# Performance work log

Hardware: AMD Instinct MI355X
Metric: run time of the kernel (lower is better)

## Reference

```python
import jax, jax.numpy as jnp
import numpy as np
import math

N, E, C, NB, NEL, NG = 8192, 131072, 64, 8, 4, 16
R_MAX, AVG_NEI, P_CUT, NL, SH = 5.0, 16.0, 6, 2, 16


def _sph(u):
    # real spherical harmonics l=0..3, component normalization (sum_m Y_lm^2 = 2l+1 on unit sphere)
    x, y, z = u[:, 0], u[:, 1], u[:, 2]
    s3, s15, s5 = math.sqrt(3.0), math.sqrt(15.0), math.sqrt(5.0)
    s105, s7 = math.sqrt(105.0), math.sqrt(7.0)
    c35, c21 = math.sqrt(35.0 / 8.0), math.sqrt(21.0 / 8.0)
    Y = [jnp.ones_like(x),
         s3 * x, s3 * y, s3 * z,
         s15 * x * y, s15 * y * z, 0.5 * s5 * (3 * z * z - 1), s15 * x * z, 0.5 * s15 * (x * x - y * y),
         c35 * y * (3 * x * x - y * y), s105 * x * y * z, c21 * y * (5 * z * z - 1),
         0.5 * s7 * (5 * z ** 3 - 3 * z), c21 * x * (5 * z * z - 1),
         0.5 * s105 * z * (x * x - y * y), c35 * x * (x * x - 3 * y * y)]
    return jnp.stack(Y, axis=-1)  # [E,16]


def _bessel(r):
    k = jnp.arange(1, NB + 1, dtype=r.dtype)
    return math.sqrt(2.0 / R_MAX) * jnp.sin(k * jnp.pi * r[:, None] / R_MAX) / r[:, None]


def _poly_cutoff(r):
    p = float(P_CUT)
    x = r / R_MAX
    f = (1.0 - 0.5 * (p + 1) * (p + 2) * x ** p + p * (p + 2) * x ** (p + 1)
         - 0.5 * p * (p + 1) * x ** (p + 2))
    return f * (x < 1.0)


def setup_inputs() -> dict:
    key = jax.random.key(0)
    ks = jax.random.split(key, 16)
    sc = lambda fan: 1.0 / math.sqrt(fan)
    return {
        "pos": 2.0 * jax.random.normal(ks[0], (N, 3), jnp.float32),
        "atom_types": jax.random.randint(ks[1], (N,), 0, NEL),
        "edge_index": jax.random.randint(ks[2], (2, E), 0, N),
        "batch": jnp.sort(jax.random.randint(ks[3], (N,), 0, NG)),
        "W_embed": jax.random.normal(ks[4], (NEL, C), jnp.float32),
        "W_r1": sc(NB) * jax.random.normal(ks[5], (NL, NB, 64), jnp.float32),
        "W_r2": sc(64) * jax.random.normal(ks[6], (NL, 64, 64), jnp.float32),
        "W_r3": sc(64) * jax.random.normal(ks[7], (NL, 64, C), jnp.float32),
        "W_sc": sc(C) * jax.random.normal(ks[8], (NL, NEL, C, C), jnp.float32),
        "w_prod": 0.5 * jax.random.normal(ks[9], (NL, NEL, 4), jnp.float32),
        "w_ro0": sc(C) * jax.random.normal(ks[10], (C,), jnp.float32),
        "W_ro1a": sc(C) * jax.random.normal(ks[11], (C, 16), jnp.float32),
        "w_ro1b": sc(16) * jax.random.normal(ks[12], (16,), jnp.float32),
    }


def reference(pos, atom_types, edge_index, batch, W_embed, W_r1, W_r2, W_r3,
              W_sc, w_prod, w_ro0, W_ro1a, w_ro1b):
    src, dst = edge_index[0], edge_index[1]
    vec = pos[dst] - pos[src]                      # [E,3]
    r = jnp.sqrt(jnp.sum(vec * vec, -1) + 1e-12)   # [E]
    Y = _sph(vec / r[:, None])                     # [E,SH]
    edge_feats = _bessel(r) * _poly_cutoff(r)[:, None]  # [E,NB]
    h = W_embed[atom_types]                        # one-hot @ W == lookup, [N,C]
    energies = [jnp.zeros((NG,), pos.dtype)]       # pair_repulsion disabled
    for i in range(NL):
        Rw = jax.nn.silu(edge_feats @ W_r1[i])
        Rw = jax.nn.silu(Rw @ W_r2[i])
        Rw = Rw @ W_r3[i]                          # radial MLP weights [E,C]
        # gather-TP-scatter: message [E,C,SH] -> node A [N,C,SH]
        m = (Rw * h[src])[:, :, None] * Y[:, None, :]
        A = jax.ops.segment_sum(m.reshape(E, C * SH), dst,
                                num_segments=N).reshape(N, C, SH) / AVG_NEI
        sc_feat = jnp.einsum('nc,ncd->nd', h, W_sc[i][atom_types])  # element-dep skip
        inv = jnp.stack([A[:, :, 0],
                         jnp.sum(A[:, :, 1:4] ** 2, -1),
                         jnp.sum(A[:, :, 4:9] ** 2, -1),
                         jnp.sum(A[:, :, 9:16] ** 2, -1)], axis=-1)  # [N,C,4]
        h = jnp.einsum('ncj,nj->nc', inv, w_prod[i][atom_types]) + sc_feat
        if i < NL - 1:
            e_node = h @ w_ro0                     # linear readout
        else:
            e_node = jax.nn.silu(h @ W_ro1a) @ w_ro1b  # gated MLP readout
        energies.append(jax.ops.segment_sum(e_node, batch, num_segments=NG))
    contributions = jnp.stack(energies, -1)        # [NG, NL+1]
    return jnp.sum(contributions, -1)              # total energy per graph
```

## Files before the change

kernel.cpp:

```cpp
#include <hip/hip_runtime.h>
#include <hip/hip_bf16.h>
#include <math.h>

#define N_NODES 8192
#define N_EDGES 131072
#define NGRP 16
#define NLAY 2
#define NELM 4
constexpr float INV_AVG = 1.0f / 16.0f;
constexpr float PI_F = 3.14159265358979323846f;

#define CV_POS   0
#define CV_EMB   24576
#define CV_SC    42240
#define CV_PROD  75008
#define CV_RO0   75040
#define CV_RO1A  75104
#define CV_RO1B  76128
#define CVT_N    76144

#define SWZ_PER_L 10240
#define SWZ_N     20480

#define B_CVT  230
#define B_SWZ  80
#define B_HIST 512
#define CVT_WORK 58736

typedef __hip_bfloat16 bf16;
typedef __attribute__((ext_vector_type(8))) short bf16x8;
typedef __attribute__((ext_vector_type(4))) float f32x4;

__device__ __forceinline__ float silu_f(float x){ return x / (1.0f + __expf(-x)); }
__device__ __forceinline__ float bfbits2f(unsigned short u){
  return __uint_as_float(((unsigned)u) << 16);
}
__device__ __forceinline__ void unpack2(unsigned u, float& lo, float& hi){
  lo = __uint_as_float(u << 16);
  hi = __uint_as_float(u & 0xffff0000u);
}
__device__ __forceinline__ short f2bs(float v){
  union { bf16 b; short s; } u; u.b = __float2bfloat16(v); return u.s;
}
__device__ __forceinline__ float ldf(const void* p, int i, int flag){
  if (flag) return bfbits2f(((const unsigned short*)p)[i]);
  return ((const float*)p)[i];
}
__device__ __forceinline__ int detect_fl(const void* pos){
  int lane = threadIdx.x & 63;
  const unsigned short* u = (const unsigned short*)pos;
  float va = bfbits2f(u[2*lane]), vb = bfbits2f(u[2*lane+1]);
  bool bad = !(fabsf(va) <= 1000.0f) || !(fabsf(vb) <= 1000.0f);
  return (__ballot(bad) == 0ull) ? 1 : 0;
}
__device__ __forceinline__ void WSYNC(){ __builtin_amdgcn_wave_barrier(); }

__device__ __forceinline__ void gl_lds4(const void* g, void* l){
  __builtin_amdgcn_global_load_lds(
      (const __attribute__((address_space(1))) unsigned*)g,
      (__attribute__((address_space(3))) unsigned*)l, 4, 0, 0);
}
__device__ __forceinline__ void gl_lds16(const void* g, void* l){
  __builtin_amdgcn_global_load_lds(
      (const __attribute__((address_space(1))) unsigned*)g,
      (__attribute__((address_space(3))) unsigned*)l, 16, 0, 0);
}

__global__ void k_setup1(const void* __restrict__ pos, const void* __restrict__ Wemb,
                         const void* __restrict__ Wsc, const void* __restrict__ wprod,
                         const void* __restrict__ wro0, const void* __restrict__ Wro1a,
                         const void* __restrict__ wro1b, const void* __restrict__ Wr1,
                         const void* __restrict__ Wr2, const void* __restrict__ Wr3,
                         const int* __restrict__ dstp, float* __restrict__ cv,
                         short* __restrict__ swz, int* __restrict__ deg){
  int b = blockIdx.x, tix = threadIdx.x;
  if (b >= B_CVT + B_SWZ){
    int e = (b - B_CVT - B_SWZ)*256 + tix;
    atomicAdd(&deg[dstp[e]], 1);
    return;
  }
  int fl = detect_fl(pos);
  if (b < B_CVT){
    int i = b*256 + tix;
    if (i < 24576){ cv[CV_POS + i] = ldf(pos, i, fl); return; }
    if (i < 24832){ int j=i-24576; cv[CV_EMB + j] = ldf(Wemb, j, fl); return; }
    if (i < 57600){ int j=i-24832; cv[CV_SC  + j] = ldf(Wsc,  j, fl); return; }
    if (i < 57632){ int j=i-57600; cv[CV_PROD+ j] = ldf(wprod,j, fl); return; }
    if (i < 57696){ int j=i-57632; cv[CV_RO0 + j] = ldf(wro0, j, fl); return; }
    if (i < 58720){ int j=i-57696; cv[CV_RO1A+ j] = ldf(Wro1a,j, fl); return; }
    if (i < CVT_WORK){ int j=i-58720; cv[CV_RO1B+ j] = ldf(wro1b,j, fl); return; }
    return;
  }
  int i = (b - B_CVT)*256 + tix;
  int l = i / SWZ_PER_L, w = i % SWZ_PER_L;
  float v;
  if (w < 2048){
    int t = w >> 9, q = (w >> 7) & 3, n = (w >> 3) & 15, j = w & 7;
    int k = q*8 + j;
    v = (k < 8) ? ldf(Wr1, l*512 + k*64 + t*16 + n, fl) : 0.0f;
  } else if (w < 6144){
    int w2 = w - 2048;
    int nt = w2 >> 10, kt = (w2 >> 9) & 1, q = (w2 >> 7) & 3, n = (w2 >> 3) & 15, j = w2 & 7;
    int k = kt*32 + q*8 + j;
    v = ldf(Wr2, l*4096 + k*64 + nt*16 + n, fl);
  } else {
    int w3 = w - 6144;
    int nt = w3 >> 10, kt = (w3 >> 9) & 1, q = (w3 >> 7) & 3, n = (w3 >> 3) & 15, j = w3 & 7;
    int k = kt*32 + q*8 + j;
    v = ldf(Wr3, l*4096 + k*64 + nt*16 + n, fl);
  }
  swz[i] = f2bs(v);
}

__global__ void k_setup2(const int* __restrict__ deg, int* __restrict__ row_start,
                         int* __restrict__ cursor, const int* __restrict__ types,
                         const float* __restrict__ cvemb, float* __restrict__ h,
                         float* __restrict__ ene){
  if (blockIdx.x == 0){
    __shared__ int lds[1024];
    int t = threadIdx.x;
    if (t < NGRP) ene[t] = 0.0f;
    int v[8]; int tot = 0;
#pragma unroll
    for (int k = 0; k < 8; k++){ v[k] = deg[t*8+k]; tot += v[k]; }
    lds[t] = tot; __syncthreads();
    for (int off = 1; off < 1024; off <<= 1){
      int x = (t >= off) ? lds[t-off] : 0;
      __syncthreads();
      lds[t] += x;
      __syncthreads();
    }
    int base = lds[t] - tot;
#pragma unroll
    for (int k = 0; k < 8; k++){ row_start[t*8+k] = base; cursor[t*8+k] = base; base += v[k]; }
    if (t == 1023) row_start[N_NODES] = base;
  } else {
    int i = (blockIdx.x - 1)*1024 + threadIdx.x;
    int n = i >> 6, c = i & 63;
    h[i] = cvemb[types[n]*64 + c];
  }
}

__global__ void k_fillgeom(const int* __restrict__ ei, int* __restrict__ cursor,
                           const float* __restrict__ posf, int* __restrict__ sslot,
                           unsigned short* __restrict__ Yb, float* __restrict__ rbuf){
  int e = blockIdx.x*256 + threadIdx.x;
  int s = ei[e], d = ei[N_EDGES + e];
  int slot = atomicAdd(&cursor[d], 1);
  sslot[slot] = s;
  float vx = posf[d*3+0] - posf[s*3+0];
  float vy = posf[d*3+1] - posf[s*3+1];
  float vz = posf[d*3+2] - posf[s*3+2];
  float r = sqrtf(vx*vx + vy*vy + vz*vz + 1e-12f);
  float ir = 1.0f / r;
  float x = vx*ir, y = vy*ir, z = vz*ir;
  const float s3 = 1.7320508075688772f, s15 = 3.872983346207417f, s5 = 2.23606797749979f;
  const float s105 = 10.246950765959598f, s7 = 2.6457513110645907f;
  const float c35 = 2.091650066335189f, c21 = 1.6201851746019651f;
  float x2 = x*x, y2 = y*y, z2 = z*z;
  float ys[16] = {
    1.0f, s3*x, s3*y, s3*z,
    s15*x*y, s15*y*z, 0.5f*s5*(3.0f*z2-1.0f), s15*x*z,
    0.5f*s15*(x2-y2), c35*y*(3.0f*x2-y2), s105*x*y*z, c21*y*(5.0f*z2-1.0f),
    0.5f*s7*(5.0f*z2*z-3.0f*z), c21*x*(5.0f*z2-1.0f), 0.5f*s105*z*(x2-y2),
    c35*x*(x2-3.0f*y2) };
  union { bf16 b[16]; uint4 u[2]; } pk;
#pragma unroll
  for (int k = 0; k < 16; k++) pk.b[k] = __float2bfloat16(ys[k]);
  uint4* yp = (uint4*)(Yb + (size_t)slot*16);
  yp[0] = pk.u[0];
  yp[1] = pk.u[1];
  rbuf[slot] = r;
}

#define ROWS 72
__global__ void __launch_bounds__(256) k_mlp2(const float* __restrict__ rbuf,
        const short* __restrict__ sw, bf16* __restrict__ Rwb){
  __shared__ short lds[4][16*ROWS];
  int tix = threadIdx.x;
  int wv = tix >> 6, lane = tix & 63;
  int q = lane >> 4, nn = lane & 15;
  int ebase = blockIdx.x*64 + wv*16;

  float r = rbuf[ebase + nn];
  float xc = r * 0.2f;
  float f = 0.0f;
  if (xc < 1.0f){
    float x3 = xc*xc*xc, x6 = x3*x3, x7 = x6*xc, x8 = x7*xc;
    f = 1.0f - 28.0f*x6 + 48.0f*x7 - 21.0f*x8;
  }
  float bs = 0.6324555320336759f * f / r;
  float t0 = PI_F * r * 0.2f;
  float ef[8];
#pragma unroll
  for (int k = 0; k < 8; k++) ef[k] = bs * __sinf((float)(k+1) * t0);

  bf16x8 af1 = {0,0,0,0,0,0,0,0};
  if (q == 0){
#pragma unroll
    for (int j = 0; j < 8; j++) af1[j] = f2bs(ef[j]);
  }
  short* A = lds[wv];
  int row = lane >> 2, c4 = lane & 3;

  for (int l = 0; l < NLAY; l++){
    const bf16x8* S1 = (const bf16x8*)(sw + l*SWZ_PER_L);
    const bf16x8* S2 = (const bf16x8*)(sw + l*SWZ_PER_L + 2048);
    const bf16x8* S3 = (const bf16x8*)(sw + l*SWZ_PER_L + 6144);
    f32x4 acc[4];
#pragma unroll
    for (int t = 0; t < 4; t++){
      bf16x8 b = S1[t*64 + q*16 + nn];
      f32x4 z = {0.f,0.f,0.f,0.f};
      acc[t] = __builtin_amdgcn_mfma_f32_16x16x32_bf16(af1, b, z, 0, 0, 0);
    }
#pragma unroll
    for (int t = 0; t < 4; t++)
#pragma unroll
      for (int rg = 0; rg < 4; rg++)
        A[(q*4+rg)*ROWS + t*16 + nn] = f2bs(silu_f(acc[t][rg]));
    WSYNC();

    bf16x8 a0 = *(const bf16x8*)&A[nn*ROWS + 0*32 + q*8];
    bf16x8 a1 = *(const bf16x8*)&A[nn*ROWS + 1*32 + q*8];
    WSYNC();
#pragma unroll
    for (int t = 0; t < 4; t++){
      f32x4 z = {0.f,0.f,0.f,0.f};
      bf16x8 b0 = S2[t*128 + 0*64 + q*16 + nn];
      bf16x8 b1 = S2[t*128 + 1*64 + q*16 + nn];
      z = __builtin_amdgcn_mfma_f32_16x16x32_bf16(a0, b0, z, 0, 0, 0);
      z = __builtin_amdgcn_mfma_f32_16x16x32_bf16(a1, b1, z, 0, 0, 0);
      acc[t] = z;
    }
#pragma unroll
    for (int t = 0; t < 4; t++)
#pragma unroll
      for (int rg = 0; rg < 4; rg++)
        A[(q*4+rg)*ROWS + t*16 + nn] = f2bs(silu_f(acc[t][rg]));
    WSYNC();

    a0 = *(const bf16x8*)&A[nn*ROWS + 0*32 + q*8];
    a1 = *(const bf16x8*)&A[nn*ROWS + 1*32 + q*8];
    WSYNC();
#pragma unroll
    for (int t = 0; t < 4; t++){
      f32x4 z = {0.f,0.f,0.f,0.f};
      bf16x8 b0 = S3[t*128 + 0*64 + q*16 + nn];
      bf16x8 b1 = S3[t*128 + 1*64 + q*16 + nn];
      z = __builtin_amdgcn_mfma_f32_16x16x32_bf16(a0, b0, z, 0, 0, 0);
      z = __builtin_amdgcn_mfma_f32_16x16x32_bf16(a1, b1, z, 0, 0, 0);
      acc[t] = z;
    }
#pragma unroll
    for (int t = 0; t < 4; t++)
#pragma unroll
      for (int rg = 0; rg < 4; rg++)
        A[(q*4+rg)*ROWS + t*16 + nn] = f2bs(acc[t][rg]);
    WSYNC();

    uint4 u0 = *(const uint4*)&A[row*ROWS + c4*16];
    uint4 u1 = *(const uint4*)&A[row*ROWS + c4*16 + 8];
    uint4* gp = (uint4*)((unsigned short*)Rwb + (size_t)l*N_EDGES*64
                         + ((size_t)(ebase + row))*64 + c4*16);
    gp[0] = u0;
    gp[1] = u1;
    WSYNC();
  }
}

template<int LAYER_KIND>
__global__ void __launch_bounds__(256) k_gu(const bf16* __restrict__ Rwb,
        const float* __restrict__ h_old, float* __restrict__ h_new,
        const unsigned short* __restrict__ Yb, const int* __restrict__ row_start,
        const int* __restrict__ sslot,
        const int* __restrict__ types, const float* __restrict__ Wsc,
        const float* __restrict__ wprod, const float* __restrict__ wro0,
        const float* __restrict__ Wro1a, const float* __restrict__ wro1b,
        const int* __restrict__ batch, float* __restrict__ ene){
  __shared__ __align__(16) float          hS[4][16][64];
  __shared__ __align__(16) unsigned short rwS[4][16][64];
  __shared__ __align__(16) unsigned short yS[4][16][16];
  __shared__ float ebins[NGRP];
  __shared__ float hn_l[4][64];
  int tix = threadIdx.x;
  if (tix < NGRP) ebins[tix] = 0.0f;
  __syncthreads();
  int wv = tix >> 6, lane = tix & 63;
  int n = blockIdx.x * 4 + wv;
  int beg = row_start[n], end = row_start[n + 1];
  const unsigned short* RW = (const unsigned short*)Rwb;

  float acc[16];
#pragma unroll
  for (int s = 0; s < 16; s++) acc[s] = 0.0f;

  for (int cb = beg; cb < end; cb += 16){
    int cnt = min(16, end - cb);
    WSYNC();
    int sv = sslot[min(cb + (lane & 15), N_EDGES - 1)];
    const char* rwsrc = (const char*)RW + (size_t)cb*128 + lane*16;
    gl_lds16(rwsrc,        &rwS[wv][0][0]);
    gl_lds16(rwsrc + 1024, &rwS[wv][8][0]);
    const char* ysrc = (const char*)Yb + (size_t)cb*32 + lane*4;
    gl_lds4(ysrc,       &yS[wv][0][0]);
    gl_lds4(ysrc + 256, &yS[wv][8][0]);
    for (int i = 0; i < cnt; i++){
      int src = __builtin_amdgcn_readlane(sv, i);
      gl_lds4(h_old + (size_t)src*64 + lane, &hS[wv][i][0]);
    }
    asm volatile("s_waitcnt vmcnt(0)" ::: "memory");
    __builtin_amdgcn_sched_barrier(0);
    for (int i = 0; i < cnt; i++){
      float g = hS[wv][i][lane] * bfbits2f(rwS[wv][i][lane]);
      const uint4* yq = (const uint4*)&yS[wv][i][0];
      uint4 ya = yq[0], yb = yq[1];
      float lo, hi;
      unpack2(ya.x, lo, hi); acc[0]  += g*lo; acc[1]  += g*hi;
      unpack2(ya.y, lo, hi); acc[2]  += g*lo; acc[3]  += g*hi;
      unpack2(ya.z, lo, hi); acc[4]  += g*lo; acc[5]  += g*hi;
      unpack2(ya.w, lo, hi); acc[6]  += g*lo; acc[7]  += g*hi;
      unpack2(yb.x, lo, hi); acc[8]  += g*lo; acc[9]  += g*hi;
      unpack2(yb.y, lo, hi); acc[10] += g*lo; acc[11] += g*hi;
      unpack2(yb.z, lo, hi); acc[12] += g*lo; acc[13] += g*hi;
      unpack2(yb.w, lo, hi); acc[14] += g*lo; acc[15] += g*hi;
    }
  }
#pragma unroll
  for (int s = 0; s < 16; s++) acc[s] *= INV_AVG;

  int ty = __builtin_amdgcn_readfirstlane(types[n]);
  const float* Ws = Wsc + (size_t)ty*4096;
  float sc0 = 0.f, sc1 = 0.f, sc2 = 0.f, sc3 = 0.f;
#pragma unroll
  for (int c = 0; c < 64; c += 4){
    sc0 += h_old[(size_t)n*64 + c+0] * Ws[(c+0)*64 + lane];
    sc1 += h_old[(size_t)n*64 + c+1] * Ws[(c+1)*64 + lane];
    sc2 += h_old[(size_t)n*64 + c+2] * Ws[(c+2)*64 + lane];
    sc3 += h_old[(size_t)n*64 + c+3] * Ws[(c+3)*64 + lane];
  }
  float sc = (sc0 + sc1) + (sc2 + sc3);

  float inv0 = acc[0];
  float inv1 = acc[1]*acc[1] + acc[2]*acc[2] + acc[3]*acc[3];
  float inv2 = acc[4]*acc[4] + acc[5]*acc[5] + acc[6]*acc[6] + acc[7]*acc[7]
             + acc[8]*acc[8];
  float inv3 = acc[9]*acc[9] + acc[10]*acc[10] + acc[11]*acc[11] + acc[12]*acc[12]
             + acc[13]*acc[13] + acc[14]*acc[14] + acc[15]*acc[15];
  const float* wp = wprod + ty*4;
  float hn = inv0*wp[0] + inv1*wp[1] + inv2*wp[2] + inv3*wp[3] + sc;
  h_new[(size_t)n*64 + lane] = hn;

  float ev;
  if (LAYER_KIND == 0){
    float p = hn * wro0[lane];
#pragma unroll
    for (int off = 32; off >= 1; off >>= 1) p += __shfl_xor(p, off, 64);
    ev = p;
  } else {
    hn_l[wv][lane] = hn;
    int j = lane & 15;
    float pj = 0.0f;
#pragma unroll
    for (int c = 0; c < 64; c++)
      pj += hn_l[wv][c] * Wro1a[c*16 + j];
    float evj = silu_f(pj) * wro1b[j];
    evj += __shfl_xor(evj, 8, 64);
    evj += __shfl_xor(evj, 4, 64);
    evj += __shfl_xor(evj, 2, 64);
    evj += __shfl_xor(evj, 1, 64);
    ev = evj;
  }
  if (lane == 0) atomicAdd(&ebins[batch[n]], ev);
  __syncthreads();
  if (tix < NGRP){
    float v = ebins[tix];
    if (v != 0.0f) atomicAdd(&ene[tix], v);
  }
}

__global__ void k_out(const float* __restrict__ ene, const void* __restrict__ pos,
                      void* __restrict__ out){
  int fl = detect_fl(pos);
  int t = threadIdx.x;
  if (t < NGRP){
    if (fl) ((bf16*)out)[t] = __float2bfloat16(ene[t]);
    else    ((float*)out)[t] = ene[t];
  }
}

static inline size_t rup(size_t x){ return (x + 255) & ~(size_t)255; }

extern "C" void kernel_launch(void* const* d_in, const int* in_sizes, int n_in,
                              void* d_out, int out_size, void* d_ws, size_t ws_size,
                              hipStream_t stream) {
  const void* pos   = d_in[0];
  const int*  types = (const int*)d_in[1];
  const int*  ei    = (const int*)d_in[2];
  const int*  batch = (const int*)d_in[3];
  const void* Wemb  = d_in[4];
  const void* Wr1   = d_in[5];
  const void* Wr2   = d_in[6];
  const void* Wr3   = d_in[7];
  const void* Wsc   = d_in[8];
  const void* wprod = d_in[9];
  const void* wro0  = d_in[10];
  const void* Wro1a = d_in[11];
  const void* wro1b = d_in[12];

  char* w = (char*)d_ws;
  float* cv       = (float*)w; w += rup((size_t)CVT_N*4);
  short* swz      = (short*)w; w += rup((size_t)SWZ_N*2);
  float* ene      = (float*)w; w += 256;
  int*   deg      = (int*)  w; w += rup((size_t)N_NODES*4);
  int*   row_start= (int*)  w; w += rup((size_t)(N_NODES+1)*4);
  int*   cursor   = (int*)  w; w += rup((size_t)N_NODES*4);
  int*   sslot    = (int*)  w; w += rup((size_t)N_EDGES*4);
  float* h0       = (float*)w; w += rup((size_t)N_NODES*64*4);
  float* h1       = (float*)w; w += rup((size_t)N_NODES*64*4);
  float* rbuf     = (float*)w; w += rup((size_t)N_EDGES*4);
  unsigned short* Yb = (unsigned short*)w; w += rup((size_t)N_EDGES*16*2);
  bf16*  Rwb      = (bf16*) w; w += rup((size_t)NLAY*N_EDGES*64*2);
  w += 4096;

  hipMemsetAsync(deg, 0, N_NODES*4, stream);

  const int* dstp = ei + N_EDGES;
  k_setup1<<<B_CVT + B_SWZ + B_HIST, 256, 0, stream>>>(
      pos, Wemb, Wsc, wprod, wro0, Wro1a, wro1b, Wr1, Wr2, Wr3, dstp, cv, swz, deg);
  k_setup2<<<1 + (N_NODES*64)/1024, 1024, 0, stream>>>(
      deg, row_start, cursor, types, cv + CV_EMB, h0, ene);
  k_fillgeom<<<N_EDGES/256, 256, 0, stream>>>(ei, cursor, cv + CV_POS, sslot, Yb, rbuf);
  k_mlp2<<<N_EDGES/64, 256, 0, stream>>>(rbuf, swz, Rwb);

  k_gu<0><<<N_NODES/4, 256, 0, stream>>>(Rwb, h0, h1, Yb,
      row_start, sslot, types, cv + CV_SC, cv + CV_PROD,
      cv + CV_RO0, cv + CV_RO1A, cv + CV_RO1B, batch, ene);
  k_gu<1><<<N_NODES/4, 256, 0, stream>>>(Rwb + (size_t)N_EDGES*64, h1, h0, Yb,
      row_start, sslot, types, cv + CV_SC + (size_t)NELM*4096, cv + CV_PROD + NELM*4,
      cv + CV_RO0, cv + CV_RO1A, cv + CV_RO1B, batch, ene);

  k_out<<<1, 64, 0, stream>>>(ene, pos, d_out);
}
```

Measured before the change: 203.0 us.

## Fuse radial MLP into gather kernels and use embeddings directly in layer 0

The separate radial-MLP kernel and its bf16 per-edge weight buffer are removed. Each k_gu wave now computes the three-layer MLP with MFMA for its 16-edge chunk into LDS, just before the gather-tensor-product loop. This avoids writing and re-reading a large per-edge intermediate. Layer 0 also skips the embedding fill kernel and the h gather: it stores per-slot source types and selects embedding rows from registers. The cost is recomputing the MLP per padded chunk, which wastes MFMA work on partial chunks, and extra register and LDS pressure in k_gu.

```diff
diff --git a/kernel.cpp b/kernel.cpp
--- a/kernel.cpp
+++ b/kernel.cpp
@@ -59,11 +59,6 @@
   __builtin_amdgcn_global_load_lds(
       (const __attribute__((address_space(1))) unsigned*)g,
       (__attribute__((address_space(3))) unsigned*)l, 4, 0, 0);
-}
-__device__ __forceinline__ void gl_lds16(const void* g, void* l){
-  __builtin_amdgcn_global_load_lds(
-      (const __attribute__((address_space(1))) unsigned*)g,
-      (__attribute__((address_space(3))) unsigned*)l, 16, 0, 0);
 }
 
 __global__ void k_setup1(const void* __restrict__ pos, const void* __restrict__ Wemb,
@@ -112,42 +107,36 @@
   swz[i] = f2bs(v);
 }
 
-__global__ void k_setup2(const int* __restrict__ deg, int* __restrict__ row_start,
-                         int* __restrict__ cursor, const int* __restrict__ types,
-                         const float* __restrict__ cvemb, float* __restrict__ h,
-                         float* __restrict__ ene){
-  if (blockIdx.x == 0){
-    __shared__ int lds[1024];
-    int t = threadIdx.x;
-    if (t < NGRP) ene[t] = 0.0f;
-    int v[8]; int tot = 0;
-#pragma unroll
-    for (int k = 0; k < 8; k++){ v[k] = deg[t*8+k]; tot += v[k]; }
-    lds[t] = tot; __syncthreads();
-    for (int off = 1; off < 1024; off <<= 1){
-      int x = (t >= off) ? lds[t-off] : 0;
-      __syncthreads();
-      lds[t] += x;
-      __syncthreads();
-    }
-    int base = lds[t] - tot;
-#pragma unroll
-    for (int k = 0; k < 8; k++){ row_start[t*8+k] = base; cursor[t*8+k] = base; base += v[k]; }
-    if (t == 1023) row_start[N_NODES] = base;
-  } else {
-    int i = (blockIdx.x - 1)*1024 + threadIdx.x;
-    int n = i >> 6, c = i & 63;
-    h[i] = cvemb[types[n]*64 + c];
-  }
+__global__ void k_scan(const int* __restrict__ deg, int* __restrict__ row_start,
+                       int* __restrict__ cursor, float* __restrict__ ene){
+  __shared__ int lds[1024];
+  int t = threadIdx.x;
+  if (t < NGRP) ene[t] = 0.0f;
+  int v[8]; int tot = 0;
+#pragma unroll
+  for (int k = 0; k < 8; k++){ v[k] = deg[t*8+k]; tot += v[k]; }
+  lds[t] = tot; __syncthreads();
+  for (int off = 1; off < 1024; off <<= 1){
+    int x = (t >= off) ? lds[t-off] : 0;
+    __syncthreads();
+    lds[t] += x;
+    __syncthreads();
+  }
+  int base = lds[t] - tot;
+#pragma unroll
+  for (int k = 0; k < 8; k++){ row_start[t*8+k] = base; cursor[t*8+k] = base; base += v[k]; }
+  if (t == 1023) row_start[N_NODES] = base;
 }
 
 __global__ void k_fillgeom(const int* __restrict__ ei, int* __restrict__ cursor,
-                           const float* __restrict__ posf, int* __restrict__ sslot,
+                           const float* __restrict__ posf, const int* __restrict__ types,
+                           int* __restrict__ sslot, unsigned char* __restrict__ tsl,
                            unsigned short* __restrict__ Yb, float* __restrict__ rbuf){
   int e = blockIdx.x*256 + threadIdx.x;
   int s = ei[e], d = ei[N_EDGES + e];
   int slot = atomicAdd(&cursor[d], 1);
   sslot[slot] = s;
+  tsl[slot] = (unsigned char)types[s];
   float vx = posf[d*3+0] - posf[s*3+0];
   float vy = posf[d*3+1] - posf[s*3+1];
   float vz = posf[d*3+2] - posf[s*3+2];
@@ -174,122 +163,38 @@
 }
 
 #define ROWS 72
-__global__ void __launch_bounds__(256) k_mlp2(const float* __restrict__ rbuf,
-        const short* __restrict__ sw, bf16* __restrict__ Rwb){
-  __shared__ short lds[4][16*ROWS];
-  int tix = threadIdx.x;
-  int wv = tix >> 6, lane = tix & 63;
-  int q = lane >> 4, nn = lane & 15;
-  int ebase = blockIdx.x*64 + wv*16;
-
-  float r = rbuf[ebase + nn];
-  float xc = r * 0.2f;
-  float f = 0.0f;
-  if (xc < 1.0f){
-    float x3 = xc*xc*xc, x6 = x3*x3, x7 = x6*xc, x8 = x7*xc;
-    f = 1.0f - 28.0f*x6 + 48.0f*x7 - 21.0f*x8;
-  }
-  float bs = 0.6324555320336759f * f / r;
-  float t0 = PI_F * r * 0.2f;
-  float ef[8];
-#pragma unroll
-  for (int k = 0; k < 8; k++) ef[k] = bs * __sinf((float)(k+1) * t0);
-
-  bf16x8 af1 = {0,0,0,0,0,0,0,0};
-  if (q == 0){
-#pragma unroll
-    for (int j = 0; j < 8; j++) af1[j] = f2bs(ef[j]);
-  }
-  short* A = lds[wv];
-  int row = lane >> 2, c4 = lane & 3;
-
-  for (int l = 0; l < NLAY; l++){
-    const bf16x8* S1 = (const bf16x8*)(sw + l*SWZ_PER_L);
-    const bf16x8* S2 = (const bf16x8*)(sw + l*SWZ_PER_L + 2048);
-    const bf16x8* S3 = (const bf16x8*)(sw + l*SWZ_PER_L + 6144);
-    f32x4 acc[4];
-#pragma unroll
-    for (int t = 0; t < 4; t++){
-      bf16x8 b = S1[t*64 + q*16 + nn];
-      f32x4 z = {0.f,0.f,0.f,0.f};
-      acc[t] = __builtin_amdgcn_mfma_f32_16x16x32_bf16(af1, b, z, 0, 0, 0);
-    }
-#pragma unroll
-    for (int t = 0; t < 4; t++)
-#pragma unroll
-      for (int rg = 0; rg < 4; rg++)
-        A[(q*4+rg)*ROWS + t*16 + nn] = f2bs(silu_f(acc[t][rg]));
-    WSYNC();
-
-    bf16x8 a0 = *(const bf16x8*)&A[nn*ROWS + 0*32 + q*8];
-    bf16x8 a1 = *(const bf16x8*)&A[nn*ROWS + 1*32 + q*8];
-    WSYNC();
-#pragma unroll
-    for (int t = 0; t < 4; t++){
-      f32x4 z = {0.f,0.f,0.f,0.f};
-      bf16x8 b0 = S2[t*128 + 0*64 + q*16 + nn];
-      bf16x8 b1 = S2[t*128 + 1*64 + q*16 + nn];
-      z = __builtin_amdgcn_mfma_f32_16x16x32_bf16(a0, b0, z, 0, 0, 0);
-      z = __builtin_amdgcn_mfma_f32_16x16x32_bf16(a1, b1, z, 0, 0, 0);
-      acc[t] = z;
-    }
-#pragma unroll
-    for (int t = 0; t < 4; t++)
-#pragma unroll
-      for (int rg = 0; rg < 4; rg++)
-        A[(q*4+rg)*ROWS + t*16 + nn] = f2bs(silu_f(acc[t][rg]));
-    WSYNC();
-
-    a0 = *(const bf16x8*)&A[nn*ROWS + 0*32 + q*8];
-    a1 = *(const bf16x8*)&A[nn*ROWS + 1*32 + q*8];
-    WSYNC();
-#pragma unroll
-    for (int t = 0; t < 4; t++){
-      f32x4 z = {0.f,0.f,0.f,0.f};
-      bf16x8 b0 = S3[t*128 + 0*64 + q*16 + nn];
-      bf16x8 b1 = S3[t*128 + 1*64 + q*16 + nn];
-      z = __builtin_amdgcn_mfma_f32_16x16x32_bf16(a0, b0, z, 0, 0, 0);
-      z = __builtin_amdgcn_mfma_f32_16x16x32_bf16(a1, b1, z, 0, 0, 0);
-      acc[t] = z;
-    }
-#pragma unroll
-    for (int t = 0; t < 4; t++)
-#pragma unroll
-      for (int rg = 0; rg < 4; rg++)
-        A[(q*4+rg)*ROWS + t*16 + nn] = f2bs(acc[t][rg]);
-    WSYNC();
-
-    uint4 u0 = *(const uint4*)&A[row*ROWS + c4*16];
-    uint4 u1 = *(const uint4*)&A[row*ROWS + c4*16 + 8];
-    uint4* gp = (uint4*)((unsigned short*)Rwb + (size_t)l*N_EDGES*64
-                         + ((size_t)(ebase + row))*64 + c4*16);
-    gp[0] = u0;
-    gp[1] = u1;
-    WSYNC();
-  }
-}
-
 template<int LAYER_KIND>
-__global__ void __launch_bounds__(256) k_gu(const bf16* __restrict__ Rwb,
-        const float* __restrict__ h_old, float* __restrict__ h_new,
-        const unsigned short* __restrict__ Yb, const int* __restrict__ row_start,
-        const int* __restrict__ sslot,
-        const int* __restrict__ types, const float* __restrict__ Wsc,
-        const float* __restrict__ wprod, const float* __restrict__ wro0,
+__global__ void __launch_bounds__(256) k_gu(const short* __restrict__ sw,
+        const float* __restrict__ rbuf, const unsigned char* __restrict__ tsl,
+        const int* __restrict__ sslot, const float* __restrict__ h_old,
+        float* __restrict__ h_new, const unsigned short* __restrict__ Yb,
+        const int* __restrict__ row_start, const int* __restrict__ types,
+        const float* __restrict__ Wsc, const float* __restrict__ wprod,
+        const float* __restrict__ wemb, const float* __restrict__ wro0,
         const float* __restrict__ Wro1a, const float* __restrict__ wro1b,
         const int* __restrict__ batch, float* __restrict__ ene){
-  __shared__ __align__(16) float          hS[4][16][64];
-  __shared__ __align__(16) unsigned short rwS[4][16][64];
+  __shared__ __align__(16) short A_[4][16*ROWS];
+  __shared__ __align__(16) float hS[LAYER_KIND ? 4 : 1][16][64];
   __shared__ __align__(16) unsigned short yS[4][16][16];
   __shared__ float ebins[NGRP];
-  __shared__ float hn_l[4][64];
+  __shared__ float hn_l[LAYER_KIND ? 4 : 1][64];
   int tix = threadIdx.x;
   if (tix < NGRP) ebins[tix] = 0.0f;
   __syncthreads();
   int wv = tix >> 6, lane = tix & 63;
+  int q = lane >> 4, nn = lane & 15;
   int n = blockIdx.x * 4 + wv;
   int beg = row_start[n], end = row_start[n + 1];
-  const unsigned short* RW = (const unsigned short*)Rwb;
+  short* A = A_[wv];
+
+  const bf16x8* S1 = (const bf16x8*)(sw);
+  const bf16x8* S2 = (const bf16x8*)(sw + 2048);
+  const bf16x8* S3 = (const bf16x8*)(sw + 6144);
+
+  float e0=0.f, e1=0.f, e2=0.f, e3=0.f;
+  if (LAYER_KIND == 0){
+    e0 = wemb[lane]; e1 = wemb[64+lane]; e2 = wemb[128+lane]; e3 = wemb[192+lane];
+  }
 
   float acc[16];
 #pragma unroll
@@ -298,21 +203,96 @@
   for (int cb = beg; cb < end; cb += 16){
     int cnt = min(16, end - cb);
     WSYNC();
-    int sv = sslot[min(cb + (lane & 15), N_EDGES - 1)];
-    const char* rwsrc = (const char*)RW + (size_t)cb*128 + lane*16;
-    gl_lds16(rwsrc,        &rwS[wv][0][0]);
-    gl_lds16(rwsrc + 1024, &rwS[wv][8][0]);
     const char* ysrc = (const char*)Yb + (size_t)cb*32 + lane*4;
     gl_lds4(ysrc,       &yS[wv][0][0]);
     gl_lds4(ysrc + 256, &yS[wv][8][0]);
-    for (int i = 0; i < cnt; i++){
-      int src = __builtin_amdgcn_readlane(sv, i);
-      gl_lds4(h_old + (size_t)src*64 + lane, &hS[wv][i][0]);
+    int tv = 0;
+    if (LAYER_KIND == 0){
+      tv = (int)tsl[min(cb + nn, N_EDGES - 1)];
+    } else {
+      int sv = sslot[min(cb + nn, N_EDGES - 1)];
+      for (int i = 0; i < cnt; i++){
+        int src = __builtin_amdgcn_readlane(sv, i);
+        gl_lds4(h_old + (size_t)src*64 + lane, &hS[wv][i][0]);
+      }
+    }
+    {
+      float r = rbuf[min(cb + nn, N_EDGES - 1)];
+      float xc = r * 0.2f;
+      float f = 0.0f;
+      if (xc < 1.0f){
+        float x3 = xc*xc*xc, x6 = x3*x3, x7 = x6*xc, x8 = x7*xc;
+        f = 1.0f - 28.0f*x6 + 48.0f*x7 - 21.0f*x8;
+      }
+      float bs = 0.6324555320336759f * f / r;
+      float t0 = PI_F * r * 0.2f;
+      bf16x8 af1 = {0,0,0,0,0,0,0,0};
+      if (q == 0){
+#pragma unroll
+        for (int j = 0; j < 8; j++) af1[j] = f2bs(bs * __sinf((float)(j+1) * t0));
+      }
+      f32x4 macc[4];
+#pragma unroll
+      for (int t = 0; t < 4; t++){
+        bf16x8 b = S1[t*64 + q*16 + nn];
+        f32x4 z = {0.f,0.f,0.f,0.f};
+        macc[t] = __builtin_amdgcn_mfma_f32_16x16x32_bf16(af1, b, z, 0, 0, 0);
+      }
+#pragma unroll
+      for (int t = 0; t < 4; t++)
+#pragma unroll
+        for (int rg = 0; rg < 4; rg++)
+          A[(q*4+rg)*ROWS + t*16 + nn] = f2bs(silu_f(macc[t][rg]));
+      WSYNC();
+      bf16x8 a0 = *(const bf16x8*)&A[nn*ROWS + 0*32 + q*8];
+      bf16x8 a1 = *(const bf16x8*)&A[nn*ROWS + 1*32 + q*8];
+      WSYNC();
+#pragma unroll
+      for (int t = 0; t < 4; t++){
+        f32x4 z = {0.f,0.f,0.f,0.f};
+        bf16x8 b0 = S2[t*128 + 0*64 + q*16 + nn];
+        bf16x8 b1 = S2[t*128 + 1*64 + q*16 + nn];
+        z = __builtin_amdgcn_mfma_f32_16x16x32_bf16(a0, b0, z, 0, 0, 0);
+        z = __builtin_amdgcn_mfma_f32_16x16x32_bf16(a1, b1, z, 0, 0, 0);
+        macc[t] = z;
+      }
+#pragma unroll
+      for (int t = 0; t < 4; t++)
+#pragma unroll
+        for (int rg = 0; rg < 4; rg++)
+          A[(q*4+rg)*ROWS + t*16 + nn] = f2bs(silu_f(macc[t][rg]));
+      WSYNC();
+      a0 = *(const bf16x8*)&A[nn*ROWS + 0*32 + q*8];
+      a1 = *(const bf16x8*)&A[nn*ROWS + 1*32 + q*8];
+      WSYNC();
+#pragma unroll
+      for (int t = 0; t < 4; t++){
+        f32x4 z = {0.f,0.f,0.f,0.f};
+        bf16x8 b0 = S3[t*128 + 0*64 + q*16 + nn];
+        bf16x8 b1 = S3[t*128 + 1*64 + q*16 + nn];
+        z = __builtin_amdgcn_mfma_f32_16x16x32_bf16(a0, b0, z, 0, 0, 0);
+        z = __builtin_amdgcn_mfma_f32_16x16x32_bf16(a1, b1, z, 0, 0, 0);
+        macc[t] = z;
+      }
+#pragma unroll
+      for (int t = 0; t < 4; t++)
+#pragma unroll
+        for (int rg = 0; rg < 4; rg++)
+          A[(q*4+rg)*ROWS + t*16 + nn] = f2bs(macc[t][rg]);
+      WSYNC();
     }
     asm volatile("s_waitcnt vmcnt(0)" ::: "memory");
     __builtin_amdgcn_sched_barrier(0);
     for (int i = 0; i < cnt; i++){
-      float g = hS[wv][i][lane] * bfbits2f(rwS[wv][i][lane]);
+      float rw = bfbits2f((unsigned short)A[i*ROWS + lane]);
+      float hv;
+      if (LAYER_KIND == 0){
+        int ty = __builtin_amdgcn_readlane(tv, i);
+        hv = (ty & 2) ? ((ty & 1) ? e3 : e2) : ((ty & 1) ? e1 : e0);
+      } else {
+        hv = hS[wv][i][lane];
+      }
+      float g = rw * hv;
       const uint4* yq = (const uint4*)&yS[wv][i][0];
       uint4 ya = yq[0], yb = yq[1];
       float lo, hi;
@@ -331,13 +311,14 @@
 
   int ty = __builtin_amdgcn_readfirstlane(types[n]);
   const float* Ws = Wsc + (size_t)ty*4096;
+  const float* hrow = (LAYER_KIND == 0) ? (wemb + ty*64) : (h_old + (size_t)n*64);
   float sc0 = 0.f, sc1 = 0.f, sc2 = 0.f, sc3 = 0.f;
 #pragma unroll
   for (int c = 0; c < 64; c += 4){
-    sc0 += h_old[(size_t)n*64 + c+0] * Ws[(c+0)*64 + lane];
-    sc1 += h_old[(size_t)n*64 + c+1] * Ws[(c+1)*64 + lane];
-    sc2 += h_old[(size_t)n*64 + c+2] * Ws[(c+2)*64 + lane];
-    sc3 += h_old[(size_t)n*64 + c+3] * Ws[(c+3)*64 + lane];
+    sc0 += hrow[c+0] * Ws[(c+0)*64 + lane];
+    sc1 += hrow[c+1] * Ws[(c+1)*64 + lane];
+    sc2 += hrow[c+2] * Ws[(c+2)*64 + lane];
+    sc3 += hrow[c+3] * Ws[(c+3)*64 + lane];
   }
   float sc = (sc0 + sc1) + (sc2 + sc3);
 
@@ -349,7 +330,8 @@
              + acc[13]*acc[13] + acc[14]*acc[14] + acc[15]*acc[15];
   const float* wp = wprod + ty*4;
   float hn = inv0*wp[0] + inv1*wp[1] + inv2*wp[2] + inv3*wp[3] + sc;
-  h_new[(size_t)n*64 + lane] = hn;
+  if (LAYER_KIND == 0)
+    h_new[(size_t)n*64 + lane] = hn;
 
   float ev;
   if (LAYER_KIND == 0){
@@ -416,11 +398,10 @@
   int*   row_start= (int*)  w; w += rup((size_t)(N_NODES+1)*4);
   int*   cursor   = (int*)  w; w += rup((size_t)N_NODES*4);
   int*   sslot    = (int*)  w; w += rup((size_t)N_EDGES*4);
-  float* h0       = (float*)w; w += rup((size_t)N_NODES*64*4);
-  float* h1       = (float*)w; w += rup((size_t)N_NODES*64*4);
+  unsigned char* tsl = (unsigned char*)w; w += rup((size_t)N_EDGES);
+  float* hbuf     = (float*)w; w += rup((size_t)N_NODES*64*4);
   float* rbuf     = (float*)w; w += rup((size_t)N_EDGES*4);
   unsigned short* Yb = (unsigned short*)w; w += rup((size_t)N_EDGES*16*2);
-  bf16*  Rwb      = (bf16*) w; w += rup((size_t)NLAY*N_EDGES*64*2);
   w += 4096;
 
   hipMemsetAsync(deg, 0, N_NODES*4, stream);
@@ -428,16 +409,17 @@
   const int* dstp = ei + N_EDGES;
   k_setup1<<<B_CVT + B_SWZ + B_HIST, 256, 0, stream>>>(
       pos, Wemb, Wsc, wprod, wro0, Wro1a, wro1b, Wr1, Wr2, Wr3, dstp, cv, swz, deg);
-  k_setup2<<<1 + (N_NODES*64)/1024, 1024, 0, stream>>>(
-      deg, row_start, cursor, types, cv + CV_EMB, h0, ene);
-  k_fillgeom<<<N_EDGES/256, 256, 0, stream>>>(ei, cursor, cv + CV_POS, sslot, Yb, rbuf);
-  k_mlp2<<<N_EDGES/64, 256, 0, stream>>>(rbuf, swz, Rwb);
-
-  k_gu<0><<<N_NODES/4, 256, 0, stream>>>(Rwb, h0, h1, Yb,
-      row_start, sslot, types, cv + CV_SC, cv + CV_PROD,
+  k_scan<<<1, 1024, 0, stream>>>(deg, row_start, cursor, ene);
+  k_fillgeom<<<N_EDGES/256, 256, 0, stream>>>(ei, cursor, cv + CV_POS, types,
+      sslot, tsl, Yb, rbuf);
+
+  k_gu<0><<<N_NODES/4, 256, 0, stream>>>(swz, rbuf, tsl, sslot,
+      hbuf , hbuf , Yb, row_start, types,
+      cv + CV_SC, cv + CV_PROD, cv + CV_EMB,
       cv + CV_RO0, cv + CV_RO1A, cv + CV_RO1B, batch, ene);
-  k_gu<1><<<N_NODES/4, 256, 0, stream>>>(Rwb + (size_t)N_EDGES*64, h1, h0, Yb,
-      row_start, sslot, types, cv + CV_SC + (size_t)NELM*4096, cv + CV_PROD + NELM*4,
+  k_gu<1><<<N_NODES/4, 256, 0, stream>>>(swz + SWZ_PER_L, rbuf, tsl, sslot,
+      hbuf , hbuf , Yb, row_start, types,
+      cv + CV_SC + (size_t)NELM*4096, cv + CV_PROD + NELM*4, cv + CV_EMB,
       cv + CV_RO0, cv + CV_RO1A, cv + CV_RO1B, batch, ene);
 
   k_out<<<1, 64, 0, stream>>>(ene, pos, d_out);
```

New measurement: 200.7 us. Within noise of the previous version (-1.2%).
